# Optimization experiments

Measured on AMD Instinct MI355X. Metric: run time of the kernel, lower is better.

## Reference

```python
import jax, jax.numpy as jnp
import numpy as np

SHARPNESS = 2


def setup_inputs() -> dict:
    key = jax.random.key(0)
    k1, k2, k3 = jax.random.split(key, 3)
    x = jax.random.normal(k1, (16, 256, 48, 48), dtype=jnp.float32)
    # 1x1 conv == per-pixel linear: weight (out_c, in_c), bias (out_c,)
    W = jax.random.normal(k2, (256, 256), dtype=jnp.float32) * 0.0625
    bias = jax.random.normal(k3, (256,), dtype=jnp.float32) * 0.01
    return {"x": x, "W": W, "bias": bias}


def reference(x, W, bias):
    b, c, h, w = x.shape
    hw = h * w
    # sample-wide L2 norm over the full (c*h*w) vector (faithful to source)
    xn = jnp.linalg.norm(x.reshape(b, -1), axis=1).reshape(b, 1, 1)
    # NOTE: raw reshapes of the (b,c,h,w)-contiguous tensor, NOT transposes
    x1 = x.reshape(b, hw, c) / xn
    x2 = x.reshape(b, c, hw) / xn
    cos = jnp.einsum('bnc,bcm->bnm', x1, x2)          # (b, hw, hw)
    s = jnp.maximum(cos, 0.0) ** SHARPNESS            # relu^sharpness
    # transform block: 1x1 conv
    tr = jnp.einsum('oc,bchw->bohw', W, x) + bias[None, :, None, None]
    tr = tr.reshape(b, hw, c)                         # raw reshape, as in source
    y = jnp.einsum('bnm,bmc->bnc', s, tr)             # (b, hw, c)
    return y.reshape(b, c, h, w)
```

## Files before the change

### kernel.cpp

```cpp
#include <hip/hip_runtime.h>

#define NB 16
#define NC 256
#define HW 2304
#define CHW 589824

typedef __attribute__((ext_vector_type(8))) short bf16x8;
typedef __attribute__((ext_vector_type(16))) float f32x16;

union BF8 { bf16x8 v; unsigned short u[8]; };

__device__ inline unsigned short f2bf(float f) {
  unsigned u = __builtin_bit_cast(unsigned, f);
  u += 0x7fffu + ((u >> 16) & 1u);
  return (unsigned short)(u >> 16);
}

__global__ __launch_bounds__(256) void prep_kernel(const float* __restrict__ x,
                                                   const float* __restrict__ W,
                                                   unsigned short* __restrict__ wp,
                                                   unsigned short* __restrict__ x1p,
                                                   unsigned short* __restrict__ xtp,
                                                   double* __restrict__ partials) {
  __shared__ __align__(16) char smem[33344];
  const int bid = blockIdx.x;
  const int tid = threadIdx.x;

  if (bid < 8) {
    const int rt = bid;
    float* tile = (float*)smem;
    const float4* src = (const float4*)(W + (size_t)rt * 32 * 256);
    #pragma unroll
    for (int it = 0; it < 8; ++it) {
      const int i = tid + 256 * it;
      float4 v = src[i];
      const int fi = 4 * i, row = fi >> 8, col = fi & 255;
      *(float4*)&tile[row * 260 + col] = v;
    }
    __syncthreads();
    const int w = tid >> 6, l = tid & 63, l31 = l & 31, h = l >> 5;
    unsigned short* dst = wp + (size_t)rt * 8192;
    #pragma unroll
    for (int ff = 0; ff < 4; ++ff) {
      const int f = 4 * w + ff;
      BF8 o;
      #pragma unroll
      for (int j = 0; j < 8; ++j)
        o.u[j] = f2bf(tile[l31 * 260 + 16 * f + 8 * h + j]);
      *(bf16x8*)(dst + (((size_t)f) * 64 + l) * 8) = o.v;
    }
  } else if (bid < 8 + 1152) {
    const int e = bid - 8;
    const int nb = e % 72, b = e / 72;
    float* tile = (float*)smem;
    double* red = (double*)(smem + 33280);
    const float4* src = (const float4*)(x + (size_t)b * CHW + nb * 8192);
    double ss = 0.0;
    #pragma unroll
    for (int it = 0; it < 8; ++it) {
      const int i = tid + 256 * it;
      float4 v = src[i];
      const int fi = 4 * i, row = fi >> 8, col = fi & 255;
      *(float4*)&tile[row * 260 + col] = v;
      ss += (double)v.x * v.x + (double)v.y * v.y + (double)v.z * v.z + (double)v.w * v.w;
    }
    #pragma unroll
    for (int off = 32; off > 0; off >>= 1) ss += __shfl_down(ss, off, 64);
    const int w = tid >> 6, l = tid & 63;
    if (l == 0) red[w] = ss;
    __syncthreads();
    if (tid == 0) partials[b * 72 + nb] = red[0] + red[1] + red[2] + red[3];
    const int l31 = l & 31, h = l >> 5;
    unsigned short* dst = x1p + (size_t)b * CHW + (size_t)nb * 8192;
    #pragma unroll
    for (int ff = 0; ff < 4; ++ff) {
      const int f = 4 * w + ff;
      BF8 o;
      #pragma unroll
      for (int j = 0; j < 8; ++j)
        o.u[j] = f2bf(tile[l31 * 260 + 16 * f + 8 * h + j]);
      *(bf16x8*)(dst + (((size_t)f) * 64 + l) * 8) = o.v;
    }
  } else {
    const int e = bid - 1160;
    const int mt = e % 36, kt = (e / 36) % 4, b = e / 144;
    const int m0 = mt * 64, k0 = kt * 64;
    float* tile = (float*)smem;
    const float* xb = x + (size_t)b * CHW;
    #pragma unroll
    for (int it = 0; it < 4; ++it) {
      const int i = tid + 256 * it;
      const int row = i >> 4, c4 = (i & 15) * 4;
      float4 v = *(const float4*)(xb + (size_t)(k0 + row) * HW + m0 + c4);
      *(float4*)&tile[row * 68 + c4] = v;
    }
    __syncthreads();
    const int w = tid >> 6, l = tid & 63, l31 = l & 31, h = l >> 5;
    unsigned short* dst = xtp + (size_t)b * CHW;
    #pragma unroll
    for (int pp = 0; pp < 2; ++pp) {
      const int p = 2 * w + pp, mbl = p >> 2, fl = p & 3;
      BF8 o;
      #pragma unroll
      for (int j = 0; j < 8; ++j)
        o.u[j] = f2bf(tile[(16 * fl + 8 * h + j) * 68 + 32 * mbl + l31]);
      const int mb = 2 * mt + mbl, f = 4 * kt + fl;
      *(bf16x8*)(dst + (((size_t)mb * 16 + f) * 64 + l) * 8) = o.v;
    }
  }
}

__global__ __launch_bounds__(256, 2) void conv_kernel(const unsigned short* __restrict__ wp,
                                                      const float* __restrict__ bias,
                                                      const unsigned short* __restrict__ xtp,
                                                      unsigned short* __restrict__ trflat,
                                                      const double* __restrict__ partials,
                                                      float* __restrict__ inv_xn2) {
  const int bid = blockIdx.x;
  if (bid == 576) {
    const int t = threadIdx.x;
    const int b = t >> 4, i0 = t & 15;
    double v = 0.0;
    for (int i = i0; i < 72; i += 16) v += partials[b * 72 + i];
    v += __shfl_down(v, 8, 64);
    v += __shfl_down(v, 4, 64);
    v += __shfl_down(v, 2, 64);
    v += __shfl_down(v, 1, 64);
    if (i0 == 0) inv_xn2[b] = (float)(1.0 / v);
    return;
  }
  const int xcd = bid & 7, j = bid >> 3;
  const int hi = (j >= 36) ? 1 : 0;
  const int b = xcd + 8 * hi;
  const int ch = j - 36 * hi;
  const int m0 = ch * 64;
  const int tid = threadIdx.x, w = tid >> 6, l = tid & 63, l31 = l & 31, h = l >> 5;
  const unsigned short* xb = xtp + (size_t)b * CHW;
  unsigned short* tb = trflat + (size_t)b * CHW;
  bf16x8 af[2][16];
  #pragma unroll
  for (int rb = 0; rb < 2; ++rb) {
    const int rt = w + 4 * rb;
    #pragma unroll
    for (int f = 0; f < 16; ++f)
      af[rb][f] = *(const bf16x8*)(wp + (((size_t)rt * 16 + f) * 64 + l) * 8);
  }
  f32x16 yacc[2][2];
  #pragma unroll
  for (int rb = 0; rb < 2; ++rb)
    #pragma unroll
    for (int cb = 0; cb < 2; ++cb)
      #pragma unroll
      for (int i = 0; i < 16; ++i) yacc[rb][cb][i] = 0.f;
  #pragma unroll 4
  for (int f = 0; f < 16; ++f) {
    #pragma unroll
    for (int cb = 0; cb < 2; ++cb) {
      const int mb = 2 * ch + cb;
      bf16x8 bv = *(const bf16x8*)(xb + (((size_t)mb * 16 + f) * 64 + l) * 8);
      yacc[0][cb] = __builtin_amdgcn_mfma_f32_32x32x16_bf16(af[0][f], bv, yacc[0][cb], 0, 0, 0);
      yacc[1][cb] = __builtin_amdgcn_mfma_f32_32x32x16_bf16(af[1][f], bv, yacc[1][cb], 0, 0, 0);
    }
  }
  #pragma unroll
  for (int rb = 0; rb < 2; ++rb)
    #pragma unroll
    for (int reg = 0; reg < 16; ++reg) {
      const int row = 32 * (w + 4 * rb) + (reg & 3) + 8 * (reg >> 2) + 4 * h;
      const float bv = bias[row];
      #pragma unroll
      for (int cb = 0; cb < 2; ++cb)
        tb[(size_t)row * HW + m0 + 32 * cb + l31] = f2bf(yacc[rb][cb][reg] + bv);
    }
}

__global__ __launch_bounds__(256) void trpack_kernel(const unsigned short* __restrict__ trflat,
                                                     unsigned short* __restrict__ trp) {
  const int mb = blockIdx.x, half = blockIdx.y, b = blockIdx.z;
  const unsigned short* src = trflat + (size_t)b * CHW + (size_t)mb * 16384 + 128 * half;
  __shared__ unsigned short tile[64 * 136];
  const int tid = threadIdx.x;
  #pragma unroll
  for (int it = 0; it < 4; ++it) {
    const int i = tid + 256 * it;
    const int row = i >> 4, c8 = (i & 15) * 8;
    *(uint4*)&tile[row * 136 + c8] = *(const uint4*)(src + (size_t)row * 256 + c8);
  }
  __syncthreads();
  const int kf = tid >> 6, l = tid & 63, l31 = l & 31, h = l >> 5;
  unsigned short* dst = trp + (size_t)b * CHW + (size_t)mb * 16384;
  #pragma unroll
  for (int cl = 0; cl < 4; ++cl) {
    BF8 o;
    #pragma unroll
    for (int j = 0; j < 8; ++j)
      o.u[j] = tile[(16 * kf + 8 * h + j) * 136 + 32 * cl + l31];
    const int cb8 = 4 * half + cl;
    *(bf16x8*)(dst + (((size_t)cb8 * 4 + kf) * 64 + l) * 8) = o.v;
  }
}

__global__ __launch_bounds__(256, 3) void fused_kernel(const unsigned short* __restrict__ x1p,
                                                       const unsigned short* __restrict__ xtp,
                                                       const unsigned short* __restrict__ trp,
                                                       const float* __restrict__ inv_xn2,
                                                       float* __restrict__ out) {
  const int bid = blockIdx.x;
  const int xcd = bid & 7, j = bid >> 3;
  const int hi = (j >= 36) ? 1 : 0;
  const int b = xcd + 8 * hi;
  const int nt = j - 36 * hi;
  const unsigned short* x1b = x1p + (size_t)b * CHW + (size_t)nt * 16384;
  const unsigned short* xtb = xtp + (size_t)b * CHW;
  const unsigned short* ttb = trp + (size_t)b * CHW;
  float* ob = out + (size_t)b * CHW;
  const float inv2 = inv_xn2[b];

  const int tid = threadIdx.x;
  const int c = tid >> 6, lane = tid & 63;
  const int l31 = lane & 31, h = lane >> 5;

  __shared__ unsigned short Af[16384];
  __shared__ unsigned short Pl[64][136];

  {
    const uint4* gsrc = (const uint4*)x1b;
    uint4* ldst = (uint4*)Af;
    #pragma unroll
    for (int it = 0; it < 8; ++it) ldst[tid + 256 * it] = gsrc[tid + 256 * it];
  }
  __syncthreads();

  f32x16 yacc[2][2];
  #pragma unroll
  for (int nh = 0; nh < 2; ++nh)
    #pragma unroll
    for (int cb = 0; cb < 2; ++cb)
      #pragma unroll
      for (int i = 0; i < 16; ++i) yacc[nh][cb][i] = 0.f;

  for (int ch = 0; ch < 18; ++ch) {
    const unsigned short* bp = xtb + ((size_t)(4 * ch + c) * 16) * 512 + lane * 8;
    f32x16 s0, s1;
    #pragma unroll
    for (int i = 0; i < 16; ++i) { s0[i] = 0.f; s1[i] = 0.f; }
    #pragma unroll
    for (int f = 0; f < 16; ++f) {
      bf16x8 bv = *(const bf16x8*)(bp + f * 512);
      bf16x8 a0 = *(const bf16x8*)(Af + (size_t)f * 512 + lane * 8);
      bf16x8 a1 = *(const bf16x8*)(Af + (size_t)(16 + f) * 512 + lane * 8);
      s0 = __builtin_amdgcn_mfma_f32_32x32x16_bf16(a0, bv, s0, 0, 0, 0);
      s1 = __builtin_amdgcn_mfma_f32_32x32x16_bf16(a1, bv, s1, 0, 0, 0);
    }
    bf16x8 bt0[8];
    #pragma unroll
    for (int kk = 0; kk < 8; ++kk) {
      const size_t mb = 2 * ch + (kk >> 2);
      bt0[kk] = *(const bf16x8*)(ttb + mb * 16384 + ((size_t)((2 * c) * 4 + (kk & 3))) * 512 + lane * 8);
    }
    __syncthreads();
    #pragma unroll
    for (int reg = 0; reg < 16; ++reg) {
      const int rowp = (reg & 3) + 8 * (reg >> 2) + 4 * h;
      float v0 = s0[reg] * inv2;
      v0 = fmaxf(v0, 0.f);
      v0 *= v0;
      float v1 = s1[reg] * inv2;
      v1 = fmaxf(v1, 0.f);
      v1 *= v1;
      Pl[rowp][32 * c + l31] = f2bf(v0);
      Pl[32 + rowp][32 * c + l31] = f2bf(v1);
    }
    __syncthreads();
    bf16x8 bt1[8];
    #pragma unroll
    for (int kk = 0; kk < 8; ++kk) {
      const size_t mb = 2 * ch + (kk >> 2);
      bt1[kk] = *(const bf16x8*)(ttb + mb * 16384 + ((size_t)((2 * c + 1) * 4 + (kk & 3))) * 512 + lane * 8);
    }
    #pragma unroll
    for (int kk = 0; kk < 8; ++kk) {
      bf16x8 pf0 = *(const bf16x8*)&Pl[l31][16 * kk + 8 * h];
      bf16x8 pf1 = *(const bf16x8*)&Pl[32 + l31][16 * kk + 8 * h];
      yacc[0][0] = __builtin_amdgcn_mfma_f32_32x32x16_bf16(pf0, bt0[kk], yacc[0][0], 0, 0, 0);
      yacc[1][0] = __builtin_amdgcn_mfma_f32_32x32x16_bf16(pf1, bt0[kk], yacc[1][0], 0, 0, 0);
    }
    #pragma unroll
    for (int kk = 0; kk < 8; ++kk) {
      bf16x8 pf0 = *(const bf16x8*)&Pl[l31][16 * kk + 8 * h];
      bf16x8 pf1 = *(const bf16x8*)&Pl[32 + l31][16 * kk + 8 * h];
      yacc[0][1] = __builtin_amdgcn_mfma_f32_32x32x16_bf16(pf0, bt1[kk], yacc[0][1], 0, 0, 0);
      yacc[1][1] = __builtin_amdgcn_mfma_f32_32x32x16_bf16(pf1, bt1[kk], yacc[1][1], 0, 0, 0);
    }
  }

  #pragma unroll
  for (int nh = 0; nh < 2; ++nh)
    #pragma unroll
    for (int cb = 0; cb < 2; ++cb) {
      const int col = 64 * c + 32 * cb + l31;
      #pragma unroll
      for (int reg = 0; reg < 16; ++reg) {
        const int rowp = (reg & 3) + 8 * (reg >> 2) + 4 * h;
        ob[(size_t)(64 * nt + 32 * nh + rowp) * NC + col] = yacc[nh][cb][reg];
      }
    }
}

extern "C" void kernel_launch(void* const* d_in, const int* in_sizes, int n_in,
                              void* d_out, int out_size, void* d_ws, size_t ws_size,
                              hipStream_t stream) {
  const float* x    = (const float*)d_in[0];
  const float* W    = (const float*)d_in[1];
  const float* bias = (const float*)d_in[2];
  float* out = (float*)d_out;

  const size_t SZ = (size_t)NB * CHW * sizeof(unsigned short);
  double* partials       = (double*)d_ws;
  float* inv_xn2         = (float*)((char*)d_ws + 16384);
  unsigned short* wp     = (unsigned short*)((char*)d_ws + 32768);
  unsigned short* x1p    = (unsigned short*)((char*)d_ws + 163840);
  unsigned short* xtp    = (unsigned short*)((char*)d_ws + 163840 + SZ);
  unsigned short* trflat = (unsigned short*)((char*)d_ws + 163840 + 2 * SZ);
  unsigned short* trp    = (unsigned short*)((char*)d_ws + 163840 + 3 * SZ);

  prep_kernel<<<3464, 256, 0, stream>>>(x, W, wp, x1p, xtp, partials);
  conv_kernel<<<577, 256, 0, stream>>>(wp, bias, xtp, trflat, partials, inv_xn2);
  trpack_kernel<<<dim3(36, 2, 16), 256, 0, stream>>>(trflat, trp);
  fused_kernel<<<576, 256, 0, stream>>>(x1p, xtp, trp, inv_xn2, out);
}
```

Measured before the change: 246.2 us.

## Software-pipeline xt loads and double-buffer the P tile in the fused kernel

The fused loop now prefetches the next chunk's xt B-fragments into registers (ping-pong bva/bvb) while the current chunk computes. It also double-buffers the P tile in LDS, which removes one of the two barriers per chunk. Both transform-tile loads are issued together before the P write. Launch bounds drop from 3 to 2 blocks per SM to make room for the extra registers and LDS, trading occupancy for latency hiding.

```diff
diff --git a/kernel.cpp b/kernel.cpp
--- a/kernel.cpp
+++ b/kernel.cpp
@@ -200,7 +200,52 @@
   }
 }
 
-__global__ __launch_bounds__(256, 3) void fused_kernel(const unsigned short* __restrict__ x1p,
+#define CHUNK_BODY(CH, CUR, NXT)                                                                   \
+  {                                                                                                \
+    const int ch_ = (CH);                                                                          \
+    const int pb_ = ch_ & 1;                                                                       \
+    f32x16 s0, s1;                                                                                 \
+    _Pragma("unroll")                                                                              \
+    for (int i = 0; i < 16; ++i) { s0[i] = 0.f; s1[i] = 0.f; }                                     \
+    _Pragma("unroll")                                                                              \
+    for (int f = 0; f < 16; ++f) {                                                                 \
+      bf16x8 a0 = *(const bf16x8*)(Af + f * 512 + lane * 8);                                       \
+      bf16x8 a1 = *(const bf16x8*)(Af + (16 + f) * 512 + lane * 8);                                \
+      s0 = __builtin_amdgcn_mfma_f32_32x32x16_bf16(a0, CUR[f], s0, 0, 0, 0);                       \
+      s1 = __builtin_amdgcn_mfma_f32_32x32x16_bf16(a1, CUR[f], s1, 0, 0, 0);                       \
+    }                                                                                              \
+    bf16x8 bt0[8], bt1[8];                                                                         \
+    _Pragma("unroll")                                                                              \
+    for (int kk = 0; kk < 8; ++kk) {                                                               \
+      const size_t mb_ = 2 * ch_ + (kk >> 2);                                                      \
+      bt0[kk] = *(const bf16x8*)(ttb + mb_ * 16384 + ((size_t)((2 * c) * 4 + (kk & 3))) * 512 + lane * 8);     \
+      bt1[kk] = *(const bf16x8*)(ttb + mb_ * 16384 + ((size_t)((2 * c + 1) * 4 + (kk & 3))) * 512 + lane * 8); \
+    }                                                                                              \
+    _Pragma("unroll")                                                                              \
+    for (int reg = 0; reg < 16; ++reg) {                                                           \
+      const int rowp = (reg & 3) + 8 * (reg >> 2) + 4 * h;                                         \
+      float v0 = fmaxf(s0[reg] * inv2, 0.f); v0 *= v0;                                             \
+      float v1 = fmaxf(s1[reg] * inv2, 0.f); v1 *= v1;                                             \
+      Pl[pb_][rowp][32 * c + l31] = f2bf(v0);                                                      \
+      Pl[pb_][32 + rowp][32 * c + l31] = f2bf(v1);                                                 \
+    }                                                                                              \
+    const int chn_ = (ch_ < 17) ? ch_ + 1 : 17;                                                    \
+    const unsigned short* bpn_ = xtb + (size_t)((4 * chn_ + c) * 16) * 512 + lane * 8;             \
+    _Pragma("unroll")                                                                              \
+    for (int f = 0; f < 16; ++f) NXT[f] = *(const bf16x8*)(bpn_ + f * 512);                        \
+    __syncthreads();                                                                               \
+    _Pragma("unroll")                                                                              \
+    for (int kk = 0; kk < 8; ++kk) {                                                               \
+      bf16x8 pf0 = *(const bf16x8*)&Pl[pb_][l31][16 * kk + 8 * h];                                 \
+      bf16x8 pf1 = *(const bf16x8*)&Pl[pb_][32 + l31][16 * kk + 8 * h];                            \
+      yacc[0][0] = __builtin_amdgcn_mfma_f32_32x32x16_bf16(pf0, bt0[kk], yacc[0][0], 0, 0, 0);     \
+      yacc[1][0] = __builtin_amdgcn_mfma_f32_32x32x16_bf16(pf1, bt0[kk], yacc[1][0], 0, 0, 0);     \
+      yacc[0][1] = __builtin_amdgcn_mfma_f32_32x32x16_bf16(pf0, bt1[kk], yacc[0][1], 0, 0, 0);     \
+      yacc[1][1] = __builtin_amdgcn_mfma_f32_32x32x16_bf16(pf1, bt1[kk], yacc[1][1], 0, 0, 0);     \
+    }                                                                                              \
+  }
+
+__global__ __launch_bounds__(256, 2) void fused_kernel(const unsigned short* __restrict__ x1p,
                                                        const unsigned short* __restrict__ xtp,
                                                        const unsigned short* __restrict__ trp,
                                                        const float* __restrict__ inv_xn2,
@@ -221,7 +266,7 @@
   const int l31 = lane & 31, h = lane >> 5;
 
   __shared__ unsigned short Af[16384];
-  __shared__ unsigned short Pl[64][136];
+  __shared__ unsigned short Pl[2][64][136];
 
   {
     const uint4* gsrc = (const uint4*)x1b;
@@ -229,6 +274,13 @@
     #pragma unroll
     for (int it = 0; it < 8; ++it) ldst[tid + 256 * it] = gsrc[tid + 256 * it];
   }
+
+  bf16x8 bva[16], bvb[16];
+  {
+    const unsigned short* bp0 = xtb + (size_t)(c * 16) * 512 + lane * 8;
+    #pragma unroll
+    for (int f = 0; f < 16; ++f) bva[f] = *(const bf16x8*)(bp0 + f * 512);
+  }
   __syncthreads();
 
   f32x16 yacc[2][2];
@@ -239,59 +291,9 @@
       #pragma unroll
       for (int i = 0; i < 16; ++i) yacc[nh][cb][i] = 0.f;
 
-  for (int ch = 0; ch < 18; ++ch) {
-    const unsigned short* bp = xtb + ((size_t)(4 * ch + c) * 16) * 512 + lane * 8;
-    f32x16 s0, s1;
-    #pragma unroll
-    for (int i = 0; i < 16; ++i) { s0[i] = 0.f; s1[i] = 0.f; }
-    #pragma unroll
-    for (int f = 0; f < 16; ++f) {
-      bf16x8 bv = *(const bf16x8*)(bp + f * 512);
-      bf16x8 a0 = *(const bf16x8*)(Af + (size_t)f * 512 + lane * 8);
-      bf16x8 a1 = *(const bf16x8*)(Af + (size_t)(16 + f) * 512 + lane * 8);
-      s0 = __builtin_amdgcn_mfma_f32_32x32x16_bf16(a0, bv, s0, 0, 0, 0);
-      s1 = __builtin_amdgcn_mfma_f32_32x32x16_bf16(a1, bv, s1, 0, 0, 0);
-    }
-    bf16x8 bt0[8];
-    #pragma unroll
-    for (int kk = 0; kk < 8; ++kk) {
-      const size_t mb = 2 * ch + (kk >> 2);
-      bt0[kk] = *(const bf16x8*)(ttb + mb * 16384 + ((size_t)((2 * c) * 4 + (kk & 3))) * 512 + lane * 8);
-    }
-    __syncthreads();
-    #pragma unroll
-    for (int reg = 0; reg < 16; ++reg) {
-      const int rowp = (reg & 3) + 8 * (reg >> 2) + 4 * h;
-      float v0 = s0[reg] * inv2;
-      v0 = fmaxf(v0, 0.f);
-      v0 *= v0;
-      float v1 = s1[reg] * inv2;
-      v1 = fmaxf(v1, 0.f);
-      v1 *= v1;
-      Pl[rowp][32 * c + l31] = f2bf(v0);
-      Pl[32 + rowp][32 * c + l31] = f2bf(v1);
-    }
-    __syncthreads();
-    bf16x8 bt1[8];
-    #pragma unroll
-    for (int kk = 0; kk < 8; ++kk) {
-      const size_t mb = 2 * ch + (kk >> 2);
-      bt1[kk] = *(const bf16x8*)(ttb + mb * 16384 + ((size_t)((2 * c + 1) * 4 + (kk & 3))) * 512 + lane * 8);
-    }
-    #pragma unroll
-    for (int kk = 0; kk < 8; ++kk) {
-      bf16x8 pf0 = *(const bf16x8*)&Pl[l31][16 * kk + 8 * h];
-      bf16x8 pf1 = *(const bf16x8*)&Pl[32 + l31][16 * kk + 8 * h];
-      yacc[0][0] = __builtin_amdgcn_mfma_f32_32x32x16_bf16(pf0, bt0[kk], yacc[0][0], 0, 0, 0);
-      yacc[1][0] = __builtin_amdgcn_mfma_f32_32x32x16_bf16(pf1, bt0[kk], yacc[1][0], 0, 0, 0);
-    }
-    #pragma unroll
-    for (int kk = 0; kk < 8; ++kk) {
-      bf16x8 pf0 = *(const bf16x8*)&Pl[l31][16 * kk + 8 * h];
-      bf16x8 pf1 = *(const bf16x8*)&Pl[32 + l31][16 * kk + 8 * h];
-      yacc[0][1] = __builtin_amdgcn_mfma_f32_32x32x16_bf16(pf0, bt1[kk], yacc[0][1], 0, 0, 0);
-      yacc[1][1] = __builtin_amdgcn_mfma_f32_32x32x16_bf16(pf1, bt1[kk], yacc[1][1], 0, 0, 0);
-    }
+  for (int ci = 0; ci < 9; ++ci) {
+    CHUNK_BODY(2 * ci, bva, bvb)
+    CHUNK_BODY(2 * ci + 1, bvb, bva)
   }
 
   #pragma unroll
```

After: 249.9 us. No clear change (+1.5%).
